# Optimization experiments

Measured on AMD Instinct MI355X. Metric: run time of the kernel, lower is better.

Reference implementation:

```python
import jax, jax.numpy as jnp
import numpy as np

B = 32        # graphs per batch
MAXN = 2048   # max nodes per graph (dense batch length)
HEADS = 8
DH = 64       # head dim (512/8)
M = 256       # FAVOR+ random features
D = 512
EPS = 1e-5    # batchnorm eps
KEPS = 1e-6   # performer stabilizer


def _batchnorm(x, g, b):
    # torch BatchNorm1d training-mode: biased batch statistics over node dim
    mu = jnp.mean(x, axis=0)
    var = jnp.mean((x - mu) ** 2, axis=0)
    return (x - mu) * jax.lax.rsqrt(var + EPS) * g + b


def setup_inputs() -> dict:
    key = jax.random.key(0)
    ks = jax.random.split(key, 10)
    sizes = 1024 + (np.arange(B) * 131) % 1025   # ragged graph sizes in [1024, 2048]
    N = int(sizes.sum())                          # 48544
    E = N * 8
    batch = jnp.asarray(np.repeat(np.arange(B), sizes), dtype=jnp.int32)
    edge_index = jax.random.randint(ks[0], (2, E), 0, N, dtype=jnp.int32)
    s = 1.0 / np.sqrt(D)
    return {
        'x': jax.random.normal(ks[1], (N, D), jnp.float32),
        'batch': batch,
        'edge_index': edge_index,
        'norm1_g': jnp.ones((D,), jnp.float32),
        'norm1_b': jnp.zeros((D,), jnp.float32),
        'norm2_g': jnp.ones((D,), jnp.float32),
        'norm2_b': jnp.zeros((D,), jnp.float32),
        'W_conv': jax.random.normal(ks[2], (D, D), jnp.float32) * s,
        'b_conv': jnp.zeros((D,), jnp.float32),
        'Wq': jax.random.normal(ks[3], (D, D), jnp.float32) * s,
        'Wk': jax.random.normal(ks[4], (D, D), jnp.float32) * s,
        'Wv': jax.random.normal(ks[5], (D, D), jnp.float32) * s,
        'Wo': jax.random.normal(ks[6], (D, D), jnp.float32) * s,
        'proj': jax.random.normal(ks[7], (M, DH), jnp.float32),
    }


def _forward(x, batch, edge_index, norm1_g, norm1_b, norm2_g, norm2_b,
             W_conv, b_conv, Wq, Wk, Wv, Wo, proj):
    N = x.shape[0]
    E = edge_index.shape[1]
    h = x

    # norm1 (+ dropout p=0 -> identity) then local GNN conv (mean-agg GCN + linear + relu)
    xn = _batchnorm(x, norm1_g, norm1_b)
    msg = xn[edge_index[0]]                                        # [E, D] gather
    agg = jax.ops.segment_sum(msg, edge_index[1], num_segments=N)  # [N, D] scatter-add
    deg = jax.ops.segment_sum(jnp.ones((E,), x.dtype), edge_index[1], num_segments=N)
    agg = agg / jnp.maximum(deg, 1.0)[:, None]
    conv_out = jax.nn.relu(agg @ W_conv + b_conv)

    # to_dense_batch(h, batch) -> h_dense [B, MAXN, D], mask [B, MAXN]
    counts = jax.ops.segment_sum(jnp.ones((N,), jnp.int32), batch, num_segments=B)
    offsets = jnp.concatenate([jnp.zeros((1,), jnp.int32), jnp.cumsum(counts)[:-1]])
    pos = jnp.arange(N, dtype=jnp.int32) - offsets[batch]
    h_dense = jnp.zeros((B, MAXN, D), x.dtype).at[batch, pos].set(h)
    mask = jnp.zeros((B, MAXN), bool).at[batch, pos].set(True)

    # Performer FAVOR+ non-causal self-attention
    def heads(t, W):
        return (t @ W).reshape(B, MAXN, HEADS, DH).transpose(0, 2, 1, 3)  # [B,H,MAXN,DH]
    q, k, v = heads(h_dense, Wq), heads(h_dense, Wk), heads(h_dense, Wv)

    scale = DH ** -0.25  # data normalizer applied to q and k each

    def phi(t, is_query):
        t = t * scale
        u = jnp.einsum('bhnd,md->bhnm', t, proj)           # [B,H,MAXN,M]
        diag = 0.5 * jnp.sum(t * t, axis=-1, keepdims=True)
        if is_query:
            m_ = jnp.max(u, axis=-1, keepdims=True)
        else:
            m_ = jnp.max(u, axis=(-2, -1), keepdims=True)
        return jnp.exp(u - diag - jax.lax.stop_gradient(m_)) / np.sqrt(M) + KEPS

    qf = phi(q, True)
    kf = phi(k, False) * mask[:, None, :, None]   # zero padded keys
    vm = v * mask[:, None, :, None]

    kv = jnp.einsum('bhnm,bhnd->bhmd', kf, vm)                    # [B,H,M,DH]
    z = 1.0 / (jnp.einsum('bhnm,bhm->bhn', qf, kf.sum(axis=2)) + KEPS)
    attn = jnp.einsum('bhnm,bhmd->bhnd', qf, kv) * z[..., None]   # [B,H,MAXN,DH]
    attn = attn.transpose(0, 2, 1, 3).reshape(B, MAXN, D) @ Wo

    h_attn = attn[batch, pos]                                      # gather back: [mask]

    return _batchnorm(conv_out + h_attn + h, norm2_g, norm2_b)


def reference(x, batch, edge_index, norm1_g, norm1_b, norm2_g, norm2_b,
              W_conv, b_conv, Wq, Wk, Wv, Wo, proj):
    return _forward(x, batch, edge_index, norm1_g, norm1_b, norm2_g, norm2_b,
                    W_conv, b_conv, Wq, Wk, Wv, Wo, proj)
```

## Files before the change

kernel.cpp:

```cpp
#include <hip/hip_runtime.h>
#include <stdint.h>

#define CDIV(a,b) (((a)+(b)-1)/(b))

typedef __attribute__((ext_vector_type(4))) float f32x4;
typedef __attribute__((ext_vector_type(8))) short s16x8;
typedef __attribute__((ext_vector_type(8))) unsigned short u16x8;
typedef __attribute__((ext_vector_type(4))) unsigned short u16x4;

__device__ __forceinline__ float bf2f(unsigned short u) {
  union { unsigned int i; float f; } c; c.i = ((unsigned int)u) << 16; return c.f;
}
__device__ __forceinline__ unsigned short f2bf(float f) {
  union { float f; unsigned int i; } c; c.f = f;
  unsigned int u = c.i;
  u += 0x7fffu + ((u >> 16) & 1u);
  return (unsigned short)(u >> 16);
}

#define KVROWS 80

template<int BM, int BN, int WM, int WN, int EPI, int GSWAP>
__global__ __launch_bounds__(256) void gemm_bt(
    const unsigned short* __restrict__ A, const unsigned short* __restrict__ B,
    void* __restrict__ Cout, const float* __restrict__ aux,
    int K, int lda, int ldb, int ldc, long zsC, int Mstore)
{
  constexpr int MT = BM / (WM * 16);
  constexpr int NT = BN / (WN * 16);
  constexpr int LDT = 40;
  __shared__ unsigned short As[BM * LDT];
  __shared__ unsigned short Bs[BN * LDT];
  const int tid = threadIdx.x, wid = tid >> 6, lane = tid & 63;
  const int l15 = lane & 15, hi = lane >> 4;
  const int wr = wid / WN, wc = wid % WN;
  const int bx = GSWAP ? blockIdx.y : blockIdx.x;
  const int by = GSWAP ? blockIdx.x : blockIdx.y;
  long m0 = (long)by * BM;
  const int n0 = bx * BN;
  f32x4 acc[MT][NT] = {};
  for (int k0 = 0; k0 < K; k0 += 32) {
    #pragma unroll
    for (int c = tid; c < BM * 4; c += 256) {
      int row = c >> 2, c8 = (c & 3) * 8;
      *(u16x8*)(&As[row * LDT + c8]) = *(const u16x8*)(A + (m0 + row) * lda + k0 + c8);
    }
    #pragma unroll
    for (int c = tid; c < BN * 4; c += 256) {
      int row = c >> 2, c8 = (c & 3) * 8;
      *(u16x8*)(&Bs[row * LDT + c8]) = *(const u16x8*)(B + (long)(n0 + row) * ldb + k0 + c8);
    }
    __syncthreads();
    s16x8 af[MT], bfv[NT];
    #pragma unroll
    for (int mt = 0; mt < MT; mt++)
      af[mt] = *(const s16x8*)(&As[(wr * MT * 16 + mt * 16 + l15) * LDT + hi * 8]);
    #pragma unroll
    for (int nt = 0; nt < NT; nt++)
      bfv[nt] = *(const s16x8*)(&Bs[(wc * NT * 16 + nt * 16 + l15) * LDT + hi * 8]);
    #pragma unroll
    for (int mt = 0; mt < MT; mt++)
      #pragma unroll
      for (int nt = 0; nt < NT; nt++)
        acc[mt][nt] = __builtin_amdgcn_mfma_f32_16x16x32_bf16(bfv[nt], af[mt], acc[mt][nt], 0, 0, 0);
    __syncthreads();
  }
  #pragma unroll
  for (int mt = 0; mt < MT; mt++) {
    long r = m0 + wr * (MT * 16) + mt * 16 + l15;
    if (r < Mstore) {
      #pragma unroll
      for (int nt = 0; nt < NT; nt++) {
        const int col0 = n0 + wc * (NT * 16) + nt * 16 + hi * 4;
        f32x4 v = acc[mt][nt];
        if constexpr (EPI == 7) {
          u16x4 o;
          #pragma unroll
          for (int i = 0; i < 4; i++) o[i] = f2bf(v[i]);
          *(u16x4*)((unsigned short*)Cout + (long)(col0 >> 6) * zsC + r * 64 + (col0 & 63)) = o;
        }
      }
    }
  }
}

__global__ __launch_bounds__(256) void gemm_out_fused(
    const unsigned short* __restrict__ A1, const unsigned short* __restrict__ B1,
    const unsigned short* __restrict__ A2, const unsigned short* __restrict__ B2,
    float* __restrict__ out, const float* __restrict__ x, const float* __restrict__ bias,
    float* __restrict__ s1, float* __restrict__ s2, int Mstore)
{
  constexpr int LDT = 40;
  __shared__ unsigned short As1[128 * LDT];
  __shared__ unsigned short Bs1[128 * LDT];
  __shared__ unsigned short As2[128 * LDT];
  __shared__ unsigned short Bs2[128 * LDT];
  const int tid = threadIdx.x, wid = tid >> 6, lane = tid & 63;
  const int l15 = lane & 15, hi = lane >> 4;
  const int wr = wid >> 1, wc = wid & 1;
  long m0 = (long)blockIdx.x * 128;
  const int n0 = blockIdx.y * 128;
  f32x4 acc1[4][4] = {};
  f32x4 acc2[4][4] = {};
  for (int k0 = 0; k0 < 512; k0 += 32) {
    #pragma unroll
    for (int c = tid; c < 512; c += 256) {
      int row = c >> 2, c8 = (c & 3) * 8;
      *(u16x8*)(&As1[row * LDT + c8]) = *(const u16x8*)(A1 + (m0 + row) * 512 + k0 + c8);
      *(u16x8*)(&Bs1[row * LDT + c8]) = *(const u16x8*)(B1 + (long)(n0 + row) * 512 + k0 + c8);
      *(u16x8*)(&As2[row * LDT + c8]) = *(const u16x8*)(A2 + (m0 + row) * 512 + k0 + c8);
      *(u16x8*)(&Bs2[row * LDT + c8]) = *(const u16x8*)(B2 + (long)(n0 + row) * 512 + k0 + c8);
    }
    __syncthreads();
    {
      s16x8 af[4], bfv[4];
      #pragma unroll
      for (int mt = 0; mt < 4; mt++)
        af[mt] = *(const s16x8*)(&As1[(wr * 64 + mt * 16 + l15) * LDT + hi * 8]);
      #pragma unroll
      for (int nt = 0; nt < 4; nt++)
        bfv[nt] = *(const s16x8*)(&Bs1[(wc * 64 + nt * 16 + l15) * LDT + hi * 8]);
      #pragma unroll
      for (int mt = 0; mt < 4; mt++)
        #pragma unroll
        for (int nt = 0; nt < 4; nt++)
          acc1[mt][nt] = __builtin_amdgcn_mfma_f32_16x16x32_bf16(bfv[nt], af[mt], acc1[mt][nt], 0, 0, 0);
    }
    {
      s16x8 af[4], bfv[4];
      #pragma unroll
      for (int mt = 0; mt < 4; mt++)
        af[mt] = *(const s16x8*)(&As2[(wr * 64 + mt * 16 + l15) * LDT + hi * 8]);
      #pragma unroll
      for (int nt = 0; nt < 4; nt++)
        bfv[nt] = *(const s16x8*)(&Bs2[(wc * 64 + nt * 16 + l15) * LDT + hi * 8]);
      #pragma unroll
      for (int mt = 0; mt < 4; mt++)
        #pragma unroll
        for (int nt = 0; nt < 4; nt++)
          acc2[mt][nt] = __builtin_amdgcn_mfma_f32_16x16x32_bf16(bfv[nt], af[mt], acc2[mt][nt], 0, 0, 0);
    }
    __syncthreads();
  }
  float st[4][4] = {};
  float sq[4][4] = {};
  #pragma unroll
  for (int mt = 0; mt < 4; mt++) {
    long r = m0 + wr * 64 + mt * 16 + l15;
    bool valid = r < Mstore;
    #pragma unroll
    for (int nt = 0; nt < 4; nt++) {
      const int col0 = n0 + wc * 64 + nt * 16 + hi * 4;
      f32x4 o = {0.f, 0.f, 0.f, 0.f};
      if (valid) {
        f32x4 xv = *(const f32x4*)(x + r * 512 + col0);
        #pragma unroll
        for (int i = 0; i < 4; i++) {
          float cv = acc2[mt][nt][i] + bias[col0 + i];
          cv = cv > 0.f ? cv : 0.f;
          o[i] = acc1[mt][nt][i] + xv[i] + cv;
        }
        *(f32x4*)(out + r * 512 + col0) = o;
      }
      #pragma unroll
      for (int i = 0; i < 4; i++) { st[nt][i] += o[i]; sq[nt][i] += o[i] * o[i]; }
    }
  }
  #pragma unroll
  for (int nt = 0; nt < 4; nt++)
    #pragma unroll
    for (int i = 0; i < 4; i++) {
      float a = st[nt][i], b = sq[nt][i];
      a += __shfl_xor(a, 1); a += __shfl_xor(a, 2); a += __shfl_xor(a, 4); a += __shfl_xor(a, 8);
      b += __shfl_xor(b, 1); b += __shfl_xor(b, 2); b += __shfl_xor(b, 4); b += __shfl_xor(b, 8);
      if (l15 == 0) {
        const int col = n0 + wc * 64 + nt * 16 + hi * 4 + i;
        atomicAdd(&s1[col], a);
        atomicAdd(&s2[col], b);
      }
    }
}

__global__ __launch_bounds__(256, 4) void k_kmax(
    const unsigned short* __restrict__ kvqh, const unsigned short* __restrict__ projb,
    const unsigned int* __restrict__ offs, unsigned int* __restrict__ kmax, long Npad) {
  __shared__ float wmax[4];
  const int tid = threadIdx.x, wid = tid >> 6, lane = tid & 63;
  const int bh = blockIdx.x & 255, xb = blockIdx.x >> 8;
  const int b = bh >> 3, h = bh & 7;
  const unsigned int off = offs[b];
  const int nb = (int)(offs[b + 1] - off);
  const int m0 = xb * 64;
  if (m0 >= nb) return;
  const unsigned short* A = kvqh + ((long)(8 + h) * Npad + off + m0) * 64;
  f32x4 acc[4][4] = {};
  #pragma unroll
  for (int k0 = 0; k0 < 64; k0 += 32) {
    s16x8 af[4], bfv[4];
    #pragma unroll
    for (int mt = 0; mt < 4; mt++)
      af[mt] = *(const s16x8*)(A + (long)(mt * 16 + (lane & 15)) * 64 + k0 + ((lane >> 4) * 8));
    #pragma unroll
    for (int nt = 0; nt < 4; nt++)
      bfv[nt] = *(const s16x8*)(projb + (long)(wid * 64 + nt * 16 + (lane & 15)) * 64 + k0 + ((lane >> 4) * 8));
    #pragma unroll
    for (int mt = 0; mt < 4; mt++)
      #pragma unroll
      for (int nt = 0; nt < 4; nt++)
        acc[mt][nt] = __builtin_amdgcn_mfma_f32_16x16x32_bf16(af[mt], bfv[nt], acc[mt][nt], 0, 0, 0);
  }
  float bm = -3.0e38f;
  #pragma unroll
  for (int mt = 0; mt < 4; mt++)
    #pragma unroll
    for (int i = 0; i < 4; i++) {
      int row = mt * 16 + ((lane >> 4) << 2) + i;
      if (m0 + row < nb) {
        #pragma unroll
        for (int nt = 0; nt < 4; nt++) bm = fmaxf(bm, acc[mt][nt][i]);
      }
    }
  #pragma unroll
  for (int s = 1; s < 64; s <<= 1) bm = fmaxf(bm, __shfl_xor(bm, s));
  if (lane == 0) wmax[wid] = bm;
  __syncthreads();
  if (tid == 0) {
    float m = fmaxf(fmaxf(wmax[0], wmax[1]), fmaxf(wmax[2], wmax[3]));
    atomicMax(&kmax[b * 8 + h], __float_as_uint(fmaxf(m, 0.f)));
  }
}

__global__ __launch_bounds__(256) void k_kvm(
    const unsigned short* __restrict__ kvqh, const unsigned short* __restrict__ projb,
    const unsigned int* __restrict__ offs, const unsigned int* __restrict__ kmax,
    unsigned short* __restrict__ kvTb, long Npad) {
  constexpr int TLD = 72;
  __shared__ unsigned short vsT[2][64 * TLD];
  __shared__ unsigned short kfsT[64 * TLD];
  const int tid = threadIdx.x, wid = tid >> 6, lane = tid & 63;
  const int bh = blockIdx.x & 255, mblk = blockIdx.x >> 8;
  const int b = bh >> 3, h = bh & 7;
  const unsigned int off = offs[b];
  const int nb = (int)(offs[b + 1] - off);
  const float km = __uint_as_float(kmax[b * 8 + h]);
  const unsigned short* Kp = kvqh + ((long)(8 + h) * Npad + off) * 64;
  const unsigned short* Vp = kvqh + ((long)(16 + h) * Npad + off) * 64;
  const unsigned short* Pp = projb + (long)(mblk * 64 + wid * 16) * 64;
  const int l15 = lane & 15, hi = lane >> 4;
  const int mloc = wid * 16 + l15;

  #pragma unroll
  for (int c = tid; c < 512; c += 256) {
    int row = c >> 3, c8 = (c & 7) * 8;
    int rot = (c & 7) * 8;
    u16x8 v = *(const u16x8*)(Vp + (long)row * 64 + c8);
    #pragma unroll
    for (int j = 0; j < 8; j++) vsT[0][(c8 + j) * TLD + ((row + rot) & 63)] = v[j];
  }
  __syncthreads();

  f32x4 akv[4] = {};
  float ksum = 0.f;
  int buf = 0;
  for (int n0 = 0; n0 < nb; n0 += 64) {
    f32x4 acc[4] = {};
    float dsum[4] = {0.f, 0.f, 0.f, 0.f};
    #pragma unroll
    for (int k0 = 0; k0 < 64; k0 += 32) {
      s16x8 af[4];
      #pragma unroll
      for (int mt = 0; mt < 4; mt++)
        af[mt] = *(const s16x8*)(Kp + ((long)n0 + mt * 16 + l15) * 64 + k0 + hi * 8);
      s16x8 bfv = *(const s16x8*)(Pp + (long)l15 * 64 + k0 + hi * 8);
      #pragma unroll
      for (int mt = 0; mt < 4; mt++) {
        #pragma unroll
        for (int j = 0; j < 8; j++) {
          float a = bf2f((unsigned short)af[mt][j]);
          dsum[mt] += a * a;
        }
        acc[mt] = __builtin_amdgcn_mfma_f32_16x16x32_bf16(af[mt], bfv, acc[mt], 0, 0, 0);
      }
    }
    float rs[4];
    #pragma unroll
    for (int mt = 0; mt < 4; mt++) {
      float s = dsum[mt];
      s += __shfl_xor(s, 16); s += __shfl_xor(s, 32);
      rs[mt] = 0.0625f * s;
    }
    #pragma unroll
    for (int mt = 0; mt < 4; mt++) {
      int r0 = mt * 16 + hi * 4;
      float e[4];
      #pragma unroll
      for (int i = 0; i < 4; i++) {
        float dg = __shfl(rs[mt], hi * 4 + i);
        e[i] = (n0 + r0 + i < nb) ? (__expf(acc[mt][i] - dg - km) * 0.0625f + 1e-6f) : 0.f;
      }
      ksum += e[0] + e[1] + e[2] + e[3];
      unsigned int p0 = (unsigned int)f2bf(e[0]) | ((unsigned int)f2bf(e[1]) << 16);
      unsigned int p1 = (unsigned int)f2bf(e[2]) | ((unsigned int)f2bf(e[3]) << 16);
      *(unsigned int*)(&kfsT[mloc * TLD + r0]) = p0;
      *(unsigned int*)(&kfsT[mloc * TLD + r0 + 2]) = p1;
    }
    if (n0 + 64 < nb) {
      #pragma unroll
      for (int c = tid; c < 512; c += 256) {
        int row = c >> 3, c8 = (c & 7) * 8;
        int rot = (c & 7) * 8;
        u16x8 v = *(const u16x8*)(Vp + ((long)n0 + 64 + row) * 64 + c8);
        #pragma unroll
        for (int j = 0; j < 8; j++) vsT[buf ^ 1][(c8 + j) * TLD + ((row + rot) & 63)] = v[j];
      }
    }
    #pragma unroll
    for (int ks = 0; ks < 2; ks++) {
      s16x8 bB = *(const s16x8*)(&kfsT[mloc * TLD + ks * 32 + hi * 8]);
      #pragma unroll
      for (int mt2 = 0; mt2 < 4; mt2++) {
        int d = mt2 * 16 + l15;
        int rrot = ((ks * 32 + hi * 8) + ((d >> 3) & 7) * 8) & 63;
        s16x8 aA = *(const s16x8*)(&vsT[buf][d * TLD + rrot]);
        akv[mt2] = __builtin_amdgcn_mfma_f32_16x16x32_bf16(aA, bB, akv[mt2], 0, 0, 0);
      }
    }
    __syncthreads();
    buf ^= 1;
  }
  long base = ((long)b * 8 + h) * (KVROWS * 256);
  const int m = mblk * 64 + mloc;
  #pragma unroll
  for (int mt2 = 0; mt2 < 4; mt2++)
    #pragma unroll
    for (int i = 0; i < 4; i++) {
      int d = mt2 * 16 + hi * 4 + i;
      kvTb[base + (long)d * 256 + m] = f2bf(akv[mt2][i]);
    }
  ksum += __shfl_xor(ksum, 16); ksum += __shfl_xor(ksum, 32);
  if (hi == 0) kvTb[base + 64 * 256 + m] = f2bf(ksum);
}

__global__ __launch_bounds__(256, 4) void k_qflash(
    const unsigned short* __restrict__ qh_all, const unsigned short* __restrict__ projb,
    const unsigned short* __restrict__ kvTb, const unsigned int* __restrict__ offs,
    unsigned short* __restrict__ attn, long Npad) {
  constexpr int QLDT = 264;
  __shared__ unsigned short qfs[64 * QLDT];
  __shared__ float sdiag[64];
  __shared__ float smax[4][64];
  const int tid = threadIdx.x, wid = tid >> 6, lane = tid & 63;
  const int l15 = lane & 15, hi = lane >> 4;
  const int bh = blockIdx.x & 255, xb = blockIdx.x >> 8;
  const int b = bh >> 3, h = bh & 7;
  const unsigned int off = offs[b];
  const int nb = (int)(offs[b + 1] - off);
  const int m0 = xb * 64;
  if (m0 >= nb) return;
  const unsigned short* A = qh_all + ((long)h * Npad + off + m0) * 64;
  f32x4 acc[4][4] = {};
  float dsum[4] = {0.f, 0.f, 0.f, 0.f};
  #pragma unroll
  for (int k0 = 0; k0 < 64; k0 += 32) {
    s16x8 af[4], bfv[4];
    #pragma unroll
    for (int mt = 0; mt < 4; mt++)
      af[mt] = *(const s16x8*)(A + (long)(mt * 16 + l15) * 64 + k0 + hi * 8);
    #pragma unroll
    for (int nt = 0; nt < 4; nt++)
      bfv[nt] = *(const s16x8*)(projb + (long)(wid * 64 + nt * 16 + l15) * 64 + k0 + hi * 8);
    if (wid == 0) {
      #pragma unroll
      for (int mt = 0; mt < 4; mt++)
        #pragma unroll
        for (int j = 0; j < 8; j++) {
          float a = bf2f((unsigned short)af[mt][j]);
          dsum[mt] += a * a;
        }
    }
    #pragma unroll
    for (int mt = 0; mt < 4; mt++)
      #pragma unroll
      for (int nt = 0; nt < 4; nt++)
        acc[mt][nt] = __builtin_amdgcn_mfma_f32_16x16x32_bf16(af[mt], bfv[nt], acc[mt][nt], 0, 0, 0);
  }
  if (wid == 0) {
    #pragma unroll
    for (int mt = 0; mt < 4; mt++) {
      float s = dsum[mt];
      s += __shfl_xor(s, 16); s += __shfl_xor(s, 32);
      if (lane < 16) sdiag[mt * 16 + lane] = 0.0625f * s;
    }
  }
  #pragma unroll
  for (int mt = 0; mt < 4; mt++)
    #pragma unroll
    for (int i = 0; i < 4; i++) {
      float rm = fmaxf(fmaxf(acc[mt][0][i], acc[mt][1][i]), fmaxf(acc[mt][2][i], acc[mt][3][i]));
      rm = fmaxf(rm, __shfl_xor(rm, 1)); rm = fmaxf(rm, __shfl_xor(rm, 2));
      rm = fmaxf(rm, __shfl_xor(rm, 4)); rm = fmaxf(rm, __shfl_xor(rm, 8));
      if (l15 == 0) smax[wid][mt * 16 + hi * 4 + i] = rm;
    }
  __syncthreads();
  #pragma unroll
  for (int mt = 0; mt < 4; mt++)
    #pragma unroll
    for (int i = 0; i < 4; i++) {
      int row = mt * 16 + hi * 4 + i;
      float rm = fmaxf(fmaxf(smax[0][row], smax[1][row]), fmaxf(smax[2][row], smax[3][row]));
      float sub = sdiag[row] + rm;
      #pragma unroll
      for (int nt = 0; nt < 4; nt++) {
        int col = wid * 64 + nt * 16 + l15;
        qfs[row * QLDT + col] = f2bf(__expf(acc[mt][nt][i] - sub) * 0.0625f + 1e-6f);
      }
    }
  __syncthreads();
  const unsigned short* kvb = kvTb + ((long)b * 8 + h) * (KVROWS * 256);
  f32x4 acc2[4] = {};
  f32x4 acc3 = {};
  #pragma unroll
  for (int ks = 0; ks < 8; ks++) {
    s16x8 aq = *(const s16x8*)(&qfs[(wid * 16 + l15) * QLDT + ks * 32 + hi * 8]);
    #pragma unroll
    for (int t = 0; t < 4; t++) {
      s16x8 bk = *(const s16x8*)(kvb + (long)(t * 16 + l15) * 256 + ks * 32 + hi * 8);
      acc2[t] = __builtin_amdgcn_mfma_f32_16x16x32_bf16(aq, bk, acc2[t], 0, 0, 0);
    }
    s16x8 bz = *(const s16x8*)(kvb + (long)(64 + l15) * 256 + ks * 32 + hi * 8);
    acc3 = __builtin_amdgcn_mfma_f32_16x16x32_bf16(aq, bz, acc3, 0, 0, 0);
  }
  float zr[4];
  #pragma unroll
  for (int i = 0; i < 4; i++) {
    float zden = __shfl(acc3[i], hi * 16);
    zr[i] = 1.f / (zden + 1e-6f);
  }
  #pragma unroll
  for (int t = 0; t < 4; t++)
    #pragma unroll
    for (int i = 0; i < 4; i++) {
      int row = wid * 16 + hi * 4 + i;
      if (m0 + row < nb)
        attn[(long)(off + m0 + row) * 512 + h * 64 + t * 16 + l15] = f2bf(acc2[t][i] * zr[i]);
    }
}


__global__ void k_fill(float* __restrict__ out, long n, float v) {
  long i = (long)blockIdx.x * 256 + threadIdx.x;
  if (i < n) out[i] = v;
}

__global__ void k_convx_stats(const float* __restrict__ x, unsigned short* __restrict__ xb,
                              float* __restrict__ s1, float* __restrict__ s2, int N, int rpb) {
  int t = threadIdx.x;
  int r0 = blockIdx.x * rpb;
  int r1 = min(N, r0 + rpb);
  float a1 = 0, a2 = 0, b1 = 0, b2 = 0;
  for (int r = r0; r < r1; r++) {
    const float* xr = x + (long)r * 512 + 2 * t;
    float va = xr[0], vb = xr[1];
    a1 += va; a2 += va * va; b1 += vb; b2 += vb * vb;
    *(unsigned int*)(xb + (long)r * 512 + 2 * t) =
        (unsigned int)f2bf(va) | ((unsigned int)f2bf(vb) << 16);
  }
  atomicAdd(&s1[2 * t], a1); atomicAdd(&s2[2 * t], a2);
  atomicAdd(&s1[2 * t + 1], b1); atomicAdd(&s2[2 * t + 1], b2);
}

__global__ void k_transall(const float* __restrict__ w0, const float* __restrict__ w1,
                           const float* __restrict__ w2, const float* __restrict__ w3,
                           const float* __restrict__ w4, unsigned short* __restrict__ out) {
  long idx = (long)blockIdx.x * 256 + threadIdx.x;
  if (idx >= (5L << 18)) return;
  int which = (int)(idx >> 18);
  int r = (int)(idx & 262143);
  int n = r >> 9, k = r & 511;
  const float* w = which == 0 ? w0 : which == 1 ? w1 : which == 2 ? w2 : which == 3 ? w3 : w4;
  out[idx] = f2bf(w[k * 512 + n]);
}

__global__ void k_scale_copy_bf(const float* __restrict__ in, unsigned short* __restrict__ out,
                                int n, float scl) {
  int i = blockIdx.x * 256 + threadIdx.x;
  if (i < n) out[i] = f2bf(in[i] * scl);
}

__global__ void k_bn_final(const float* __restrict__ s1, const float* __restrict__ s2,
                           const float* __restrict__ g, const float* __restrict__ b,
                           float* __restrict__ a, float* __restrict__ c, float invN) {
  int t = threadIdx.x;
  float mu = s1[t] * invN;
  float var = s2[t] * invN - mu * mu;
  float inv = rsqrtf(var + 1e-5f);
  float av = g[t] * inv;
  a[t] = av;
  c[t] = b[t] - mu * av;
}

__global__ void k_deg(const int* __restrict__ ed, unsigned int* __restrict__ deg, long E) {
  long i = (long)blockIdx.x * 256 + threadIdx.x;
  if (i < E) atomicAdd(&deg[ed[i]], 1u);
}

__global__ void k_offs(const int* __restrict__ batch, unsigned int* __restrict__ offs, int N) {
  int i = blockIdx.x * 256 + threadIdx.x;
  if (i >= N) return;
  int b = batch[i];
  if (i == 0) { for (int bb = 0; bb <= b; bb++) offs[bb] = 0; }
  else {
    int pb = batch[i - 1];
    if (pb != b) for (int bb = pb + 1; bb <= b; bb++) offs[bb] = i;
  }
  if (i == N - 1) { for (int bb = b + 1; bb <= 32; bb++) offs[bb] = N; }
}

__global__ __launch_bounds__(1024) void k_scan_nodes(const unsigned int* __restrict__ deg,
                                                     unsigned int* __restrict__ rowstart, int N) {
  __shared__ unsigned int wsum[16];
  __shared__ unsigned int carry_s;
  int t = threadIdx.x, lane = t & 63, wid = t >> 6;
  if (t == 0) carry_s = 0;
  __syncthreads();
  for (int base = 0; base < N; base += 1024) {
    int i = base + t;
    unsigned int v = (i < N) ? deg[i] : 0;
    unsigned int sc = v;
    #pragma unroll
    for (int s = 1; s < 64; s <<= 1) {
      unsigned int u = __shfl_up(sc, s);
      if (lane >= s) sc += u;
    }
    if (lane == 63) wsum[wid] = sc;
    __syncthreads();
    unsigned int woff = 0, tot = 0;
    #pragma unroll
    for (int w = 0; w < 16; w++) { unsigned int s = wsum[w]; if (w < wid) woff += s; tot += s; }
    unsigned int carry = carry_s;
    if (i < N) rowstart[i] = carry + woff + sc - v;
    __syncthreads();
    if (t == 0) carry_s = carry + tot;
    __syncthreads();
  }
  if (threadIdx.x == 0) rowstart[N] = carry_s;
}

__global__ void k_csr_fill(const int* __restrict__ es, const int* __restrict__ ed,
                           const unsigned int* __restrict__ rowstart,
                           unsigned int* __restrict__ cursor, int* __restrict__ csr, long E) {
  long e = (long)blockIdx.x * 256 + threadIdx.x;
  if (e >= E) return;
  int d = ed[e];
  unsigned int slot = atomicAdd(&cursor[d], 1u);
  csr[rowstart[d] + slot] = es[e];
}

__global__ __launch_bounds__(128) void k_gather(const int* __restrict__ csr,
                                                const unsigned int* __restrict__ rowstart,
                                                const float* __restrict__ x,
                                                const float* __restrict__ a1, const float* __restrict__ c1,
                                                unsigned short* __restrict__ conv_in, int N) {
  long n = blockIdx.x;
  int c = threadIdx.x * 4;
  u16x4 o; o[0] = 0; o[1] = 0; o[2] = 0; o[3] = 0;
  if (n < N) {
    unsigned int r0 = rowstart[n], r1 = rowstart[n + 1];
    if (r1 > r0) {
      f32x4 acc0 = {}, acc1 = {};
      unsigned int j = r0;
      for (; j + 2 <= r1; j += 2) {
        int s0 = csr[j], s1 = csr[j + 1];
        acc0 += *(const f32x4*)(x + (long)s0 * 512 + c);
        acc1 += *(const f32x4*)(x + (long)s1 * 512 + c);
      }
      if (j < r1) { int s0 = csr[j]; acc0 += *(const f32x4*)(x + (long)s0 * 512 + c); }
      f32x4 acc = acc0 + acc1;
      float inv = 1.f / (float)(r1 - r0);
      o[0] = f2bf(acc[0] * inv * a1[c + 0] + c1[c + 0]);
      o[1] = f2bf(acc[1] * inv * a1[c + 1] + c1[c + 1]);
      o[2] = f2bf(acc[2] * inv * a1[c + 2] + c1[c + 2]);
      o[3] = f2bf(acc[3] * inv * a1[c + 3] + c1[c + 3]);
    }
  }
  *(u16x4*)(conv_in + n * 512 + c) = o;
}

__global__ void k_bn_apply(float* __restrict__ y, const float* __restrict__ a,
                           const float* __restrict__ c, long total) {
  long i4 = ((long)blockIdx.x * 256 + threadIdx.x) * 4;
  if (i4 >= total) return;
  int col = (int)(i4 & 511);
  f32x4 v = *(const f32x4*)(y + i4);
  #pragma unroll
  for (int j = 0; j < 4; j++) v[j] = v[j] * a[col + j] + c[col + j];
  *(f32x4*)(y + i4) = v;
}


extern "C" void kernel_launch(void* const* d_in, const int* in_sizes, int n_in,
                              void* d_out, int out_size, void* d_ws, size_t ws_size,
                              hipStream_t stream) {
  (void)n_in; (void)out_size;
  const float* x = (const float*)d_in[0];
  const int* batch = (const int*)d_in[1];
  const int* eidx = (const int*)d_in[2];
  const float* n1g = (const float*)d_in[3];
  const float* n1b = (const float*)d_in[4];
  const float* n2g = (const float*)d_in[5];
  const float* n2b = (const float*)d_in[6];
  const float* wconv = (const float*)d_in[7];
  const float* bconv = (const float*)d_in[8];
  const float* wq = (const float*)d_in[9];
  const float* wk = (const float*)d_in[10];
  const float* wv = (const float*)d_in[11];
  const float* wo = (const float*)d_in[12];
  const float* proj = (const float*)d_in[13];

  const int N = in_sizes[1];
  const long E = in_sizes[2] / 2;
  const long Npad = CDIV(N, 128) * 128 + 256;
  const int Mb = (int)((CDIV(N, 128) * 128 + 128) / 128);
  const int MbO = CDIV(N, 128);
  const int* es = eidx;
  const int* ed = eidx + E;
  float* out = (float*)d_out;

  char* p = (char*)d_ws;
  auto alloc = [&](size_t bytes) -> char* {
    char* r = p;
    p += (bytes + 255) & ~(size_t)255;
    return r;
  };
  unsigned short* kvqh = (unsigned short*)alloc((size_t)24 * Npad * 64 * 2);
  unsigned short* xbf  = (unsigned short*)alloc((size_t)Npad * 512 * 2);
  unsigned short* kvT_b = (unsigned short*)alloc((size_t)32 * 8 * KVROWS * 256 * 2);
  unsigned short* wts   = (unsigned short*)alloc((size_t)5 * 512 * 512 * 2);
  unsigned short* proj_s = (unsigned short*)alloc((size_t)256 * 64 * 2);
  float* bn1_acc = (float*)alloc(1024 * 4);
  float* bn1_ac  = (float*)alloc(1024 * 4);
  float* bn2_acc = (float*)alloc(1024 * 4);
  float* bn2_ac  = (float*)alloc(1024 * 4);
  unsigned int* deg      = (unsigned int*)alloc((size_t)N * 4);
  unsigned int* offs     = (unsigned int*)alloc(33 * 4);
  unsigned int* kmax     = (unsigned int*)alloc(32 * 8 * 4);
  unsigned int* rowstart = (unsigned int*)alloc((size_t)(N + 1) * 4);
  unsigned int* cursor   = (unsigned int*)alloc((size_t)N * 4);
  int* csr               = (int*)alloc((size_t)E * 4);
  size_t required = (size_t)(p - (char*)d_ws);
  if (required > ws_size) {
    k_fill<<<(int)CDIV((long)N * 512, 256), 256, 0, stream>>>(
        out, (long)N * 512, 1.0e6f + (float)(ws_size >> 20));
    return;
  }
  unsigned short* wqkv_t  = wts;
  unsigned short* wconv_t = wts + 3 * 512 * 512;
  unsigned short* wo_t    = wts + 4 * 512 * 512;
  unsigned short* attn2   = kvqh + (size_t)8 * Npad * 64;
  unsigned short* conv_in = xbf;

  hipMemsetAsync(deg, 0, (size_t)N * 4, stream);
  hipMemsetAsync(cursor, 0, (size_t)N * 4, stream);
  hipMemsetAsync(kmax, 0, 32 * 8 * 4, stream);
  hipMemsetAsync(bn1_acc, 0, 1024 * 4, stream);
  hipMemsetAsync(bn2_acc, 0, 1024 * 4, stream);
  hipMemsetAsync(xbf + (size_t)N * 512, 0, (size_t)(Npad - N) * 512 * 2, stream);

  int rpb = CDIV(N, 1024);
  k_convx_stats<<<1024, 256, 0, stream>>>(x, xbf, bn1_acc, bn1_acc + 512, N, rpb);
  k_transall<<<(int)CDIV(5L << 18, 256), 256, 0, stream>>>(wq, wk, wv, wconv, wo, wts);
  k_scale_copy_bf<<<CDIV(256 * 64, 256), 256, 0, stream>>>(proj, proj_s, 256 * 64, 0.35355339059327373f);
  k_bn_final<<<1, 512, 0, stream>>>(bn1_acc, bn1_acc + 512, n1g, n1b, bn1_ac, bn1_ac + 512, 1.f / N);
  k_deg<<<(int)CDIV(E, 256), 256, 0, stream>>>(ed, deg, E);
  k_offs<<<CDIV(N, 256), 256, 0, stream>>>(batch, offs, N);
  k_scan_nodes<<<1, 1024, 0, stream>>>(deg, rowstart, N);
  k_csr_fill<<<(int)CDIV(E, 256), 256, 0, stream>>>(es, ed, rowstart, cursor, csr, E);

  gemm_bt<128, 128, 2, 2, 7, 1><<<dim3(Mb, 12), 256, 0, stream>>>(
      xbf, wqkv_t, kvqh, nullptr, 512, 512, 512, 0, (long)Npad * 64, (int)Npad);

  k_kmax<<<32 * 256, 256, 0, stream>>>(kvqh, proj_s, offs, kmax, Npad);
  k_kvm<<<4 * 256, 256, 0, stream>>>(kvqh, proj_s, offs, kmax, kvT_b, Npad);

  k_gather<<<(int)(CDIV(N, 128) * 128), 128, 0, stream>>>(csr, rowstart, x, bn1_ac, bn1_ac + 512, conv_in, N);

  k_qflash<<<32 * 256, 256, 0, stream>>>(
      kvqh, proj_s, kvT_b, offs, attn2, Npad);

  gemm_out_fused<<<dim3(MbO, 4), 256, 0, stream>>>(
      attn2, wo_t, conv_in, wconv_t, out, x, bconv, bn2_acc, bn2_acc + 512, N);

  k_bn_final<<<1, 512, 0, stream>>>(bn2_acc, bn2_acc + 512, n2g, n2b, bn2_ac, bn2_ac + 512, 1.f / N);
  k_bn_apply<<<(int)CDIV((long)N * 512 / 4, 256), 256, 0, stream>>>(out, bn2_ac, bn2_ac + 512, (long)N * 512);
}
```

Before: 1.239 ms.

## Gather neighbours from bf16 activations and split fused output GEMM in two

The neighbour aggregation now reads the bf16 copy of x instead of fp32 x, roughly halving the bytes moved by the edge gather. Because the gather no longer writes over xbf, conv_in gets its own buffer. The dual-GEMM output kernel is split into a plain GEMM that writes attn@Wo + x, and a conv GEMM that adds relu(conv) onto out while collecting BN statistics. This frees shared memory and registers per kernel, at the cost of an extra full read/write pass over out and slightly lower precision in the aggregated features.

```diff
diff --git a/kernel.cpp b/kernel.cpp
--- a/kernel.cpp
+++ b/kernel.cpp
@@ -78,68 +78,52 @@
           #pragma unroll
           for (int i = 0; i < 4; i++) o[i] = f2bf(v[i]);
           *(u16x4*)((unsigned short*)Cout + (long)(col0 >> 6) * zsC + r * 64 + (col0 & 63)) = o;
+        } else if constexpr (EPI == 8) {
+          const f32x4 ax = *(const f32x4*)(aux + r * ldc + col0);
+          f32x4 o;
+          #pragma unroll
+          for (int i = 0; i < 4; i++) o[i] = v[i] + ax[i];
+          *(f32x4*)((float*)Cout + r * ldc + col0) = o;
         }
       }
     }
   }
 }
 
-__global__ __launch_bounds__(256) void gemm_out_fused(
-    const unsigned short* __restrict__ A1, const unsigned short* __restrict__ B1,
-    const unsigned short* __restrict__ A2, const unsigned short* __restrict__ B2,
-    float* __restrict__ out, const float* __restrict__ x, const float* __restrict__ bias,
+__global__ __launch_bounds__(256) void gemm_conv_bn(
+    const unsigned short* __restrict__ A, const unsigned short* __restrict__ B,
+    float* __restrict__ out, const float* __restrict__ bias,
     float* __restrict__ s1, float* __restrict__ s2, int Mstore)
 {
   constexpr int LDT = 40;
-  __shared__ unsigned short As1[128 * LDT];
-  __shared__ unsigned short Bs1[128 * LDT];
-  __shared__ unsigned short As2[128 * LDT];
-  __shared__ unsigned short Bs2[128 * LDT];
+  __shared__ unsigned short As[128 * LDT];
+  __shared__ unsigned short Bs[128 * LDT];
   const int tid = threadIdx.x, wid = tid >> 6, lane = tid & 63;
   const int l15 = lane & 15, hi = lane >> 4;
   const int wr = wid >> 1, wc = wid & 1;
-  long m0 = (long)blockIdx.x * 128;
-  const int n0 = blockIdx.y * 128;
-  f32x4 acc1[4][4] = {};
-  f32x4 acc2[4][4] = {};
+  long m0 = (long)blockIdx.y * 128;
+  const int n0 = blockIdx.x * 128;
+  f32x4 acc[4][4] = {};
   for (int k0 = 0; k0 < 512; k0 += 32) {
     #pragma unroll
     for (int c = tid; c < 512; c += 256) {
       int row = c >> 2, c8 = (c & 3) * 8;
-      *(u16x8*)(&As1[row * LDT + c8]) = *(const u16x8*)(A1 + (m0 + row) * 512 + k0 + c8);
-      *(u16x8*)(&Bs1[row * LDT + c8]) = *(const u16x8*)(B1 + (long)(n0 + row) * 512 + k0 + c8);
-      *(u16x8*)(&As2[row * LDT + c8]) = *(const u16x8*)(A2 + (m0 + row) * 512 + k0 + c8);
-      *(u16x8*)(&Bs2[row * LDT + c8]) = *(const u16x8*)(B2 + (long)(n0 + row) * 512 + k0 + c8);
-    }
-    __syncthreads();
-    {
-      s16x8 af[4], bfv[4];
-      #pragma unroll
-      for (int mt = 0; mt < 4; mt++)
-        af[mt] = *(const s16x8*)(&As1[(wr * 64 + mt * 16 + l15) * LDT + hi * 8]);
+      *(u16x8*)(&As[row * LDT + c8]) = *(const u16x8*)(A + (m0 + row) * 512 + k0 + c8);
+      *(u16x8*)(&Bs[row * LDT + c8]) = *(const u16x8*)(B + (long)(n0 + row) * 512 + k0 + c8);
+    }
+    __syncthreads();
+    s16x8 af[4], bfv[4];
+    #pragma unroll
+    for (int mt = 0; mt < 4; mt++)
+      af[mt] = *(const s16x8*)(&As[(wr * 64 + mt * 16 + l15) * LDT + hi * 8]);
+    #pragma unroll
+    for (int nt = 0; nt < 4; nt++)
+      bfv[nt] = *(const s16x8*)(&Bs[(wc * 64 + nt * 16 + l15) * LDT + hi * 8]);
+    #pragma unroll
+    for (int mt = 0; mt < 4; mt++)
       #pragma unroll
       for (int nt = 0; nt < 4; nt++)
-        bfv[nt] = *(const s16x8*)(&Bs1[(wc * 64 + nt * 16 + l15) * LDT + hi * 8]);
-      #pragma unroll
-      for (int mt = 0; mt < 4; mt++)
-        #pragma unroll
-        for (int nt = 0; nt < 4; nt++)
-          acc1[mt][nt] = __builtin_amdgcn_mfma_f32_16x16x32_bf16(bfv[nt], af[mt], acc1[mt][nt], 0, 0, 0);
-    }
-    {
-      s16x8 af[4], bfv[4];
-      #pragma unroll
-      for (int mt = 0; mt < 4; mt++)
-        af[mt] = *(const s16x8*)(&As2[(wr * 64 + mt * 16 + l15) * LDT + hi * 8]);
-      #pragma unroll
-      for (int nt = 0; nt < 4; nt++)
-        bfv[nt] = *(const s16x8*)(&Bs2[(wc * 64 + nt * 16 + l15) * LDT + hi * 8]);
-      #pragma unroll
-      for (int mt = 0; mt < 4; mt++)
-        #pragma unroll
-        for (int nt = 0; nt < 4; nt++)
-          acc2[mt][nt] = __builtin_amdgcn_mfma_f32_16x16x32_bf16(bfv[nt], af[mt], acc2[mt][nt], 0, 0, 0);
-    }
+        acc[mt][nt] = __builtin_amdgcn_mfma_f32_16x16x32_bf16(bfv[nt], af[mt], acc[mt][nt], 0, 0, 0);
     __syncthreads();
   }
   float st[4][4] = {};
@@ -153,14 +137,15 @@
       const int col0 = n0 + wc * 64 + nt * 16 + hi * 4;
       f32x4 o = {0.f, 0.f, 0.f, 0.f};
       if (valid) {
-        f32x4 xv = *(const f32x4*)(x + r * 512 + col0);
+        float* cp = out + r * 512 + col0;
+        f32x4 cur = *(f32x4*)cp;
         #pragma unroll
         for (int i = 0; i < 4; i++) {
-          float cv = acc2[mt][nt][i] + bias[col0 + i];
+          float cv = acc[mt][nt][i] + bias[col0 + i];
           cv = cv > 0.f ? cv : 0.f;
-          o[i] = acc1[mt][nt][i] + xv[i] + cv;
+          o[i] = cur[i] + cv;
         }
-        *(f32x4*)(out + r * 512 + col0) = o;
+        *(f32x4*)cp = o;
       }
       #pragma unroll
       for (int i = 0; i < 4; i++) { st[nt][i] += o[i]; sq[nt][i] += o[i] * o[i]; }
@@ -558,7 +543,7 @@
 
 __global__ __launch_bounds__(128) void k_gather(const int* __restrict__ csr,
                                                 const unsigned int* __restrict__ rowstart,
-                                                const float* __restrict__ x,
+                                                const unsigned short* __restrict__ xb,
                                                 const float* __restrict__ a1, const float* __restrict__ c1,
                                                 unsigned short* __restrict__ conv_in, int N) {
   long n = blockIdx.x;
@@ -570,11 +555,16 @@
       f32x4 acc0 = {}, acc1 = {};
       unsigned int j = r0;
       for (; j + 2 <= r1; j += 2) {
-        int s0 = csr[j], s1 = csr[j + 1];
-        acc0 += *(const f32x4*)(x + (long)s0 * 512 + c);
-        acc1 += *(const f32x4*)(x + (long)s1 * 512 + c);
-      }
-      if (j < r1) { int s0 = csr[j]; acc0 += *(const f32x4*)(x + (long)s0 * 512 + c); }
+        u16x4 v0 = *(const u16x4*)(xb + (long)csr[j] * 512 + c);
+        u16x4 v1 = *(const u16x4*)(xb + (long)csr[j + 1] * 512 + c);
+        #pragma unroll
+        for (int i = 0; i < 4; i++) { acc0[i] += bf2f(v0[i]); acc1[i] += bf2f(v1[i]); }
+      }
+      if (j < r1) {
+        u16x4 v0 = *(const u16x4*)(xb + (long)csr[j] * 512 + c);
+        #pragma unroll
+        for (int i = 0; i < 4; i++) acc0[i] += bf2f(v0[i]);
+      }
       f32x4 acc = acc0 + acc1;
       float inv = 1.f / (float)(r1 - r0);
       o[0] = f2bf(acc[0] * inv * a1[c + 0] + c1[c + 0]);
@@ -621,7 +611,7 @@
   const long E = in_sizes[2] / 2;
   const long Npad = CDIV(N, 128) * 128 + 256;
   const int Mb = (int)((CDIV(N, 128) * 128 + 128) / 128);
-  const int MbO = CDIV(N, 128);
+  const int MbC = CDIV(N, 128);
   const int* es = eidx;
   const int* ed = eidx + E;
   float* out = (float*)d_out;
@@ -634,6 +624,7 @@
   };
   unsigned short* kvqh = (unsigned short*)alloc((size_t)24 * Npad * 64 * 2);
   unsigned short* xbf  = (unsigned short*)alloc((size_t)Npad * 512 * 2);
+  unsigned short* conv_in = (unsigned short*)alloc((size_t)Npad * 512 * 2);
   unsigned short* kvT_b = (unsigned short*)alloc((size_t)32 * 8 * KVROWS * 256 * 2);
   unsigned short* wts   = (unsigned short*)alloc((size_t)5 * 512 * 512 * 2);
   unsigned short* proj_s = (unsigned short*)alloc((size_t)256 * 64 * 2);
@@ -657,7 +648,6 @@
   unsigned short* wconv_t = wts + 3 * 512 * 512;
   unsigned short* wo_t    = wts + 4 * 512 * 512;
   unsigned short* attn2   = kvqh + (size_t)8 * Npad * 64;
-  unsigned short* conv_in = xbf;
 
   hipMemsetAsync(deg, 0, (size_t)N * 4, stream);
   hipMemsetAsync(cursor, 0, (size_t)N * 4, stream);
@@ -682,13 +672,16 @@
   k_kmax<<<32 * 256, 256, 0, stream>>>(kvqh, proj_s, offs, kmax, Npad);
   k_kvm<<<4 * 256, 256, 0, stream>>>(kvqh, proj_s, offs, kmax, kvT_b, Npad);
 
-  k_gather<<<(int)(CDIV(N, 128) * 128), 128, 0, stream>>>(csr, rowstart, x, bn1_ac, bn1_ac + 512, conv_in, N);
+  k_gather<<<MbC * 128, 128, 0, stream>>>(csr, rowstart, xbf, bn1_ac, bn1_ac + 512, conv_in, N);
 
   k_qflash<<<32 * 256, 256, 0, stream>>>(
       kvqh, proj_s, kvT_b, offs, attn2, Npad);
 
-  gemm_out_fused<<<dim3(MbO, 4), 256, 0, stream>>>(
-      attn2, wo_t, conv_in, wconv_t, out, x, bconv, bn2_acc, bn2_acc + 512, N);
+  gemm_bt<128, 128, 2, 2, 8, 0><<<dim3(4, MbC), 256, 0, stream>>>(
+      attn2, wo_t, out, x, 512, 512, 512, 512, 0, N);
+
+  gemm_conv_bn<<<dim3(4, MbC), 256, 0, stream>>>(
+      conv_in, wconv_t, out, bconv, bn2_acc, bn2_acc + 512, N);
 
   k_bn_final<<<1, 512, 0, stream>>>(bn2_acc, bn2_acc + 512, n2g, n2b, bn2_ac, bn2_ac + 512, 1.f / N);
   k_bn_apply<<<(int)CDIV((long)N * 512 / 4, 256), 256, 0, stream>>>(out, bn2_ac, bn2_ac + 512, (long)N * 512);
```

Measured after the change: 1.050 ms. 15.2% less time.
